# Optimization experiments

Hardware: AMD Instinct MI355X
Metric: run time of the kernel (lower is better)

Reference implementation:

```python
import jax, jax.numpy as jnp
import numpy as np

STRIDE = (1, 1)
PAD = (1, 1)

def setup_inputs() -> dict:
    key = jax.random.key(0)
    k1, k2, k3 = jax.random.split(key, 3)
    x = jax.random.normal(k1, (32, 128, 56, 56), dtype=jnp.float32)
    # K ~ N(0,1) per nn.init.normal_(self.K)
    K = jax.random.normal(k2, (256, 128, 3, 3), dtype=jnp.float32)
    bias = jax.random.normal(k3, (1,), dtype=jnp.float32)  # single scalar bias added to whole output
    return {"x": x, "K": K, "bias": bias}

def reference(x, K, bias):
    # Cross-correlation (torch conv semantics), NCHW / OIHW, zero padding.
    y = jax.lax.conv_general_dilated(
        x, K,
        window_strides=STRIDE,
        padding=[(PAD[0], PAD[0]), (PAD[1], PAD[1])],
        dimension_numbers=("NCHW", "OIHW", "NCHW"),
    )
    # Original adds a single scalar bias to the entire output tensor.
    return y + bias
```

## Files before the change

kernel.cpp:

```cpp
#include <hip/hip_runtime.h>

typedef __bf16 bf16x8 __attribute__((ext_vector_type(8)));
typedef float  floatx16 __attribute__((ext_vector_type(16)));

#define HW   56
#define NPIX 3136
#define CIN  128
#define COUT 256

#define AS_GLOBAL __attribute__((address_space(1)))
#define AS_LDS    __attribute__((address_space(3)))

__global__ __launch_bounds__(256) void wt_transform_kernel(
        const float* __restrict__ Kw, __bf16* __restrict__ W2) {
    int idx = blockIdx.x * 256 + threadIdx.x;
    int j     = idx & 7;
    int oc    = (idx >> 3) & 255;
    int cg    = (idx >> 11) & 3;
    int tapcc = idx >> 13;
    int tap   = tapcc % 9;
    int cc    = tapcc / 9;
    int c = cc * 32 + cg * 8 + j;
    W2[idx] = (__bf16)Kw[oc * 1152 + c * 9 + tap];
}

__device__ __forceinline__ int xs_idx(int row, int wp, int cg) {
    return row * 2640 + wp * 40 + cg * 8;
}

__global__ __launch_bounds__(512, 4) void conv_kernel(
        const float* __restrict__ x, const __bf16* __restrict__ W2,
        const float* __restrict__ bias, float* __restrict__ out) {
    __shared__ __align__(16) __bf16 Xs[6 * 2640];
    __shared__ __align__(16) __bf16 Abuf[2][3 * 4096];

    const int t    = threadIdx.x;
    const int nb   = blockIdx.x / 14;
    const int ht   = blockIdx.x % 14;
    const int h0   = ht * 4;
    const int ocb  = blockIdx.y * 128;

    const int wid  = t >> 6;
    const int lane = t & 63;
    const int half = lane >> 5;
    const int l31  = lane & 31;

    const int oc_rel = (wid & 1) * 64;
    const int prow   = wid >> 1;
    const int aocc   = (oc_rel + l31) * 8;

    floatx16 acc[2][2];
    #pragma unroll
    for (int mi = 0; mi < 2; ++mi)
        #pragma unroll
        for (int nj = 0; nj < 2; ++nj)
            #pragma unroll
            for (int k = 0; k < 16; ++k)
                acc[mi][nj][k] = 0.f;

    if (t < 240) {
        int cg   = t & 3;
        int rest = t >> 2;
        int row  = rest / 10;
        int zw   = rest % 10;
        int wp   = (zw == 0) ? 0 : (56 + zw);
        *(int4*)&Xs[xs_idx(row, wp, cg)] = make_int4(0, 0, 0, 0);
    }

    auto dma_a = [&](int cc, int tap, int buf, int slot) {
        const __bf16* src = W2 + (size_t)(cc * 9 + tap) * 8192
                          + (t >> 7) * 2048 + (size_t)(ocb + (t & 127)) * 8;
        __builtin_amdgcn_global_load_lds(
            (const AS_GLOBAL unsigned*)(const void*)src,
            (AS_LDS unsigned*)(void*)&Abuf[buf][slot * 4096 + t * 8], 16, 0, 0);
    };

    auto compute_group = [&](int g, int b) {
        __builtin_amdgcn_s_setprio(1);
        #pragma unroll
        for (int tp = 0; tp < 3; ++tp) {
            const __bf16* At = &Abuf[b][tp * 4096];
            #pragma unroll
            for (int kc = 0; kc < 2; ++kc) {
                bf16x8 afr[2];
                #pragma unroll
                for (int mi = 0; mi < 2; ++mi)
                    afr[mi] = *(const bf16x8*)&At[(kc * 2 + half) * 1024 + aocc + mi * 256];
                bf16x8 bfr[2];
                #pragma unroll
                for (int nj = 0; nj < 2; ++nj)
                    bfr[nj] = *(const bf16x8*)&Xs[xs_idx(prow + g, nj * 32 + l31 + tp,
                                                         kc * 2 + half)];
                #pragma unroll
                for (int mi = 0; mi < 2; ++mi)
                    #pragma unroll
                    for (int nj = 0; nj < 2; ++nj)
                        acc[mi][nj] = __builtin_amdgcn_mfma_f32_32x32x16_bf16(
                            afr[mi], bfr[nj], acc[mi][nj], 0, 0, 0);
            }
        }
        __builtin_amdgcn_s_setprio(0);
    };

    const int  sw     = t & 63;
    const int  sgr    = t >> 6;
    const int  sg     = sgr & 3;
    const int  rg2    = sgr >> 2;
    const bool wvalid = sw < 56;

    for (int cc = 0; cc < 4; ++cc) {
        __syncthreads();
        #pragma unroll
        for (int tp = 0; tp < 3; ++tp) dma_a(cc, tp, 0, tp);
        if (cc == 0) {
            #pragma unroll
            for (int tp = 0; tp < 3; ++tp) dma_a(0, 3 + tp, 1, tp);
        }
        #pragma unroll
        for (int p = 0; p < 3; ++p) {
            int row = rg2 * 3 + p;
            int hin = h0 - 1 + row;
            bf16x8 v;
            #pragma unroll
            for (int j = 0; j < 8; ++j) v[j] = (__bf16)0.f;
            if (wvalid && (unsigned)hin < 56u) {
                const float* src = x + (size_t)(nb * CIN + cc * 32 + sg * 8) * NPIX
                                     + hin * HW + sw;
                #pragma unroll
                for (int j = 0; j < 8; ++j)
                    v[j] = (__bf16)src[j * NPIX];
            }
            if (wvalid)
                *(bf16x8*)&Xs[xs_idx(row, 1 + sw, sg)] = v;
        }
        __syncthreads();

        compute_group(0, 0);

        __builtin_amdgcn_s_barrier();
        #pragma unroll
        for (int tp = 0; tp < 3; ++tp) dma_a(cc, 6 + tp, 0, tp);

        compute_group(1, 1);

        asm volatile("s_waitcnt vmcnt(0)" ::: "memory");
        __builtin_amdgcn_s_barrier();
        if (cc < 3) {
            #pragma unroll
            for (int tp = 0; tp < 3; ++tp) dma_a(cc + 1, 3 + tp, 1, tp);
        }

        compute_group(2, 0);
    }

    const float bv = bias[0];
    const int hout = h0 + prow;
    const int oc_base = ocb + oc_rel;
    #pragma unroll
    for (int nj = 0; nj < 2; ++nj) {
        int pw = nj * 32 + l31;
        if (pw < 56) {
            #pragma unroll
            for (int mi = 0; mi < 2; ++mi) {
                #pragma unroll
                for (int rg = 0; rg < 16; ++rg) {
                    int oc = oc_base + mi * 32 + (rg & 3) + ((rg >> 2) << 3) + half * 4;
                    out[(size_t)(nb * COUT + oc) * NPIX + hout * HW + pw] = acc[mi][nj][rg] + bv;
                }
            }
        }
    }
}

extern "C" void kernel_launch(void* const* d_in, const int* in_sizes, int n_in,
                              void* d_out, int out_size, void* d_ws, size_t ws_size,
                              hipStream_t stream) {
    const float* x    = (const float*)d_in[0];
    const float* Kw   = (const float*)d_in[1];
    const float* bias = (const float*)d_in[2];
    float* out = (float*)d_out;
    __bf16* W2 = (__bf16*)d_ws;

    wt_transform_kernel<<<dim3(1152), dim3(256), 0, stream>>>(Kw, W2);
    conv_kernel<<<dim3(32 * 14, 2), dim3(512), 0, stream>>>(x, W2, bias, out);
}
```

Before: 192.5 us.

## Double-buffer input tile and stream weights per tap to overlap loads with MFMA

Restructures the main loop into a per-tap software pipeline. Each tap's weight slice is fetched with a double-buffered async global-to-LDS load issued one tap ahead. The next channel chunk's input rows are prefetched into registers in stages across taps and written into a second LDS input buffer. This targets the serialized input staging and barrier stalls that sat between channel chunks. In exchange there is a barrier per tap, hand-tuned vmcnt waits that must match the outstanding load counts, and two input tile copies in LDS, which may affect occupancy.

```diff
diff --git a/kernel.cpp b/kernel.cpp
--- a/kernel.cpp
+++ b/kernel.cpp
@@ -31,8 +31,8 @@
 __global__ __launch_bounds__(512, 4) void conv_kernel(
         const float* __restrict__ x, const __bf16* __restrict__ W2,
         const float* __restrict__ bias, float* __restrict__ out) {
-    __shared__ __align__(16) __bf16 Xs[6 * 2640];
-    __shared__ __align__(16) __bf16 Abuf[2][3 * 4096];
+    __shared__ __align__(16) __bf16 Xs[2][6 * 2640];
+    __shared__ __align__(16) __bf16 Abuf[2][4096];
 
     const int t    = threadIdx.x;
     const int nb   = blockIdx.x / 14;
@@ -64,42 +64,16 @@
         int row  = rest / 10;
         int zw   = rest % 10;
         int wp   = (zw == 0) ? 0 : (56 + zw);
-        *(int4*)&Xs[xs_idx(row, wp, cg)] = make_int4(0, 0, 0, 0);
-    }
-
-    auto dma_a = [&](int cc, int tap, int buf, int slot) {
-        const __bf16* src = W2 + (size_t)(cc * 9 + tap) * 8192
+        *(int4*)&Xs[0][xs_idx(row, wp, cg)] = make_int4(0, 0, 0, 0);
+        *(int4*)&Xs[1][xs_idx(row, wp, cg)] = make_int4(0, 0, 0, 0);
+    }
+
+    auto dma_a = [&](int g, int buf) {
+        const __bf16* src = W2 + (size_t)g * 8192
                           + (t >> 7) * 2048 + (size_t)(ocb + (t & 127)) * 8;
         __builtin_amdgcn_global_load_lds(
             (const AS_GLOBAL unsigned*)(const void*)src,
-            (AS_LDS unsigned*)(void*)&Abuf[buf][slot * 4096 + t * 8], 16, 0, 0);
-    };
-
-    auto compute_group = [&](int g, int b) {
-        __builtin_amdgcn_s_setprio(1);
-        #pragma unroll
-        for (int tp = 0; tp < 3; ++tp) {
-            const __bf16* At = &Abuf[b][tp * 4096];
-            #pragma unroll
-            for (int kc = 0; kc < 2; ++kc) {
-                bf16x8 afr[2];
-                #pragma unroll
-                for (int mi = 0; mi < 2; ++mi)
-                    afr[mi] = *(const bf16x8*)&At[(kc * 2 + half) * 1024 + aocc + mi * 256];
-                bf16x8 bfr[2];
-                #pragma unroll
-                for (int nj = 0; nj < 2; ++nj)
-                    bfr[nj] = *(const bf16x8*)&Xs[xs_idx(prow + g, nj * 32 + l31 + tp,
-                                                         kc * 2 + half)];
-                #pragma unroll
-                for (int mi = 0; mi < 2; ++mi)
-                    #pragma unroll
-                    for (int nj = 0; nj < 2; ++nj)
-                        acc[mi][nj] = __builtin_amdgcn_mfma_f32_32x32x16_bf16(
-                            afr[mi], bfr[nj], acc[mi][nj], 0, 0, 0);
-            }
-        }
-        __builtin_amdgcn_s_setprio(0);
+            (AS_LDS unsigned*)(void*)&Abuf[buf][t * 8], 16, 0, 0);
     };
 
     const int  sw     = t & 63;
@@ -107,50 +81,103 @@
     const int  sg     = sgr & 3;
     const int  rg2    = sgr >> 2;
     const bool wvalid = sw < 56;
+    const int  swc    = sw < 55 ? sw : 55;
+
+    #pragma unroll
+    for (int p = 0; p < 3; ++p) {
+        int row = rg2 * 3 + p;
+        int hin = h0 - 1 + row;
+        bf16x8 v;
+        #pragma unroll
+        for (int j = 0; j < 8; ++j) v[j] = (__bf16)0.f;
+        if (wvalid && (unsigned)hin < 56u) {
+            const float* src = x + (size_t)(nb * CIN + sg * 8) * NPIX + hin * HW + sw;
+            #pragma unroll
+            for (int j = 0; j < 8; ++j)
+                v[j] = (__bf16)src[j * NPIX];
+        }
+        if (wvalid)
+            *(bf16x8*)&Xs[0][xs_idx(row, 1 + sw, sg)] = v;
+    }
+    dma_a(0, 0);
+    __syncthreads();
 
     for (int cc = 0; cc < 4; ++cc) {
-        __syncthreads();
+        const __bf16* Xcur = &Xs[cc & 1][0];
+        __bf16*       Xoth = &Xs[(cc & 1) ^ 1][0];
+        const bool do_stg = (cc < 3);
+        const float* sx = x + (size_t)(nb * CIN + (cc + 1) * 32 + sg * 8) * NPIX;
+
+        float sreg[8];
+
         #pragma unroll
-        for (int tp = 0; tp < 3; ++tp) dma_a(cc, tp, 0, tp);
-        if (cc == 0) {
-            #pragma unroll
-            for (int tp = 0; tp < 3; ++tp) dma_a(0, 3 + tp, 1, tp);
+        for (int tap = 0; tap < 9; ++tap) {
+            const int g = cc * 9 + tap;
+
+            if (tap == 0) {
+                if (cc > 0) {
+                    asm volatile("s_waitcnt vmcnt(0) lgkmcnt(0)" ::: "memory");
+                    __builtin_amdgcn_s_barrier();
+                }
+            } else {
+                if (do_stg && (tap == 3 || tap == 5 || tap == 7))
+                    asm volatile("s_waitcnt vmcnt(8)" ::: "memory");
+                else
+                    asm volatile("s_waitcnt vmcnt(0)" ::: "memory");
+                __builtin_amdgcn_s_barrier();
+            }
+
+            if (do_stg && (tap == 3 || tap == 5 || tap == 7)) {
+                const int p   = (tap - 3) / 2;
+                const int row = rg2 * 3 + p;
+                const int hin = h0 - 1 + row;
+                const bool hv = (unsigned)hin < 56u;
+                bf16x8 v;
+                #pragma unroll
+                for (int j = 0; j < 8; ++j)
+                    v[j] = (__bf16)(hv ? sreg[j] : 0.f);
+                if (wvalid)
+                    *(bf16x8*)&Xoth[xs_idx(row, 1 + sw, sg)] = v;
+            }
+
+            if (g < 35) dma_a(g + 1, (g + 1) & 1);
+
+            if (do_stg && (tap == 2 || tap == 4 || tap == 6)) {
+                const int p   = (tap - 2) / 2;
+                const int row = rg2 * 3 + p;
+                const int hin = h0 - 1 + row;
+                const int hc  = hin < 0 ? 0 : (hin > 55 ? 55 : hin);
+                const float* srcp = sx + hc * HW + swc;
+                #pragma unroll
+                for (int j = 0; j < 8; ++j)
+                    sreg[j] = srcp[j * NPIX];
+            }
+
+            {
+                const int r = tap / 3, s = tap % 3;
+                const __bf16* At = &Abuf[g & 1][0];
+                __builtin_amdgcn_s_setprio(1);
+                #pragma unroll
+                for (int kc = 0; kc < 2; ++kc) {
+                    bf16x8 afr[2];
+                    #pragma unroll
+                    for (int mi = 0; mi < 2; ++mi)
+                        afr[mi] = *(const bf16x8*)&At[(kc * 2 + half) * 1024 + aocc + mi * 256];
+                    bf16x8 bfr[2];
+                    #pragma unroll
+                    for (int nj = 0; nj < 2; ++nj)
+                        bfr[nj] = *(const bf16x8*)&Xcur[xs_idx(prow + r, nj * 32 + l31 + s,
+                                                               kc * 2 + half)];
+                    #pragma unroll
+                    for (int mi = 0; mi < 2; ++mi)
+                        #pragma unroll
+                        for (int nj = 0; nj < 2; ++nj)
+                            acc[mi][nj] = __builtin_amdgcn_mfma_f32_32x32x16_bf16(
+                                afr[mi], bfr[nj], acc[mi][nj], 0, 0, 0);
+                }
+                __builtin_amdgcn_s_setprio(0);
+            }
         }
-        #pragma unroll
-        for (int p = 0; p < 3; ++p) {
-            int row = rg2 * 3 + p;
-            int hin = h0 - 1 + row;
-            bf16x8 v;
-            #pragma unroll
-            for (int j = 0; j < 8; ++j) v[j] = (__bf16)0.f;
-            if (wvalid && (unsigned)hin < 56u) {
-                const float* src = x + (size_t)(nb * CIN + cc * 32 + sg * 8) * NPIX
-                                     + hin * HW + sw;
-                #pragma unroll
-                for (int j = 0; j < 8; ++j)
-                    v[j] = (__bf16)src[j * NPIX];
-            }
-            if (wvalid)
-                *(bf16x8*)&Xs[xs_idx(row, 1 + sw, sg)] = v;
-        }
-        __syncthreads();
-
-        compute_group(0, 0);
-
-        __builtin_amdgcn_s_barrier();
-        #pragma unroll
-        for (int tp = 0; tp < 3; ++tp) dma_a(cc, 6 + tp, 0, tp);
-
-        compute_group(1, 1);
-
-        asm volatile("s_waitcnt vmcnt(0)" ::: "memory");
-        __builtin_amdgcn_s_barrier();
-        if (cc < 3) {
-            #pragma unroll
-            for (int tp = 0; tp < 3; ++tp) dma_a(cc + 1, 3 + tp, 1, tp);
-        }
-
-        compute_group(2, 0);
     }
 
     const float bv = bias[0];
```

Result: slower. 200.7 us (+4.3%).
